# Performance work log

Measured on AMD Instinct MI355X. Metric: run time of the kernel, lower is better.

## Reference

```python
import jax, jax.numpy as jnp
import numpy as np

H, W = 200, 200            # image_size
X_RANGE = (0.0, 100.0)
Y_RANGE = (0.0, 100.0)
SIZE = 36                   # kernel 'size' from source
SIGMA = 3.0
K = SIZE + 1                # kernel is 37x37 (arange(-18, 19))


def _gaussian_kernel():
    r = jnp.arange(-(SIZE // 2), SIZE // 2 + 1, dtype=jnp.float32)
    k1 = jnp.exp(-(r ** 2) / (2.0 * SIGMA ** 2))
    k2 = k1[:, None] * k1[None, :]
    return k2 / k2.sum()    # [K, K]


def setup_inputs() -> dict:
    key = jax.random.key(0)
    # trajectory coords in world units [0, 100) -> spread over whole map
    x_t = jax.random.uniform(key, (512, 64, 2), dtype=jnp.float32) * 100.0
    return {"x_t": x_t}


def reference(x_t):
    B, T, _ = x_t.shape
    x_scale = W / (X_RANGE[1] - X_RANGE[0])
    y_scale = H / (Y_RANGE[1] - Y_RANGE[0])
    # .long() in torch truncates toward zero; inputs are >= 0 here so astype(int32) matches
    x_pix = ((x_t[:, :, 0] - X_RANGE[0]) * x_scale).astype(jnp.int32)   # [B, T]
    y_pix = H - ((x_t[:, :, 1] - Y_RANGE[0]) * y_scale).astype(jnp.int32)
    valid = ~(jnp.isnan(x_t[:, :, 0]) | jnp.isnan(x_t[:, :, 1]))        # [B, T]

    half = SIZE // 2
    x_start = jnp.clip(x_pix - half, 0, W - SIZE)
    y_start = jnp.clip(y_pix - half, 0, H - SIZE)
    x_end = jnp.clip(x_pix + half, 0, W)
    y_end = jnp.clip(y_pix + half, 0, H)
    kx = x_end - x_start    # patch width  (<= 36, kernel[:,:kx] = top-left slice)
    ky = y_end - y_start    # patch height

    kern = _gaussian_kernel()                       # [K, K]
    r = jnp.arange(K)
    c = jnp.arange(K)
    # mask: kernel[:ky, :kx] slice, and point validity            [B, T, K, K]
    mask = ((r[None, None, :, None] < ky[..., None, None])
            & (c[None, None, None, :] < kx[..., None, None])
            & valid[..., None, None])
    vals = jnp.where(mask, kern[None, None, :, :], 0.0)            # [B, T, K, K]
    rows = jnp.clip(y_start[..., None, None] + r[None, None, :, None], 0, H - 1)
    cols = jnp.clip(x_start[..., None, None] + c[None, None, None, :], 0, W - 1)
    rows = jnp.broadcast_to(rows, (B, T, K, K))
    cols = jnp.broadcast_to(cols, (B, T, K, K))
    flat = (rows * W + cols).reshape(B, -1)                        # [B, T*K*K]

    # parallel scatter-add splat of all Gaussian patches
    heat = jnp.zeros((B, H * W), jnp.float32)
    heat = heat.at[jnp.arange(B)[:, None], flat].add(vals.reshape(B, -1))
    heat = heat.reshape(B, H, W)

    # per-image max normalization (max over dim1 then dim2 == max over both)
    m = heat.max(axis=(1, 2), keepdims=True)
    return heat / (m + 1e-10)
```

## Files before the change

### kernel.cpp

```cpp
#include <hip/hip_runtime.h>


#define NT 64
#define BLK 512
#define TDIM 224
#define NTL 7

typedef short bf16x8 __attribute__((ext_vector_type(8)));
typedef float f32x16 __attribute__((ext_vector_type(16)));

static __device__ inline unsigned short f2bf(float f) {
    unsigned int u = __float_as_uint(f);
    u = (u + 0x7FFFu + ((u >> 16) & 1u)) >> 16;
    return (unsigned short)u;
}

struct __align__(16) SMem {
    unsigned short Rm[TDIM][64];
    unsigned short Cm[TDIM][64];
    unsigned short k1b[40];
    float wmax[8];
};

__global__ __launch_bounds__(BLK, 4) void heatmap_kernel(const float* __restrict__ x_t,
                                                         float* __restrict__ out) {
    __shared__ SMem s;
    const int tid  = threadIdx.x;
    const int lane = tid & 63;
    const int wv   = tid >> 6;
    const int b    = blockIdx.x;

    if (tid < 37) {
        float sum = 0.0f, mine = 0.0f;
        #pragma unroll
        for (int i = 0; i < 37; ++i) {
            float r = (float)(i - 18);
            float v = expf(-(r * r) * (1.0f / 18.0f));
            sum += v;
            if (i == tid) mine = v;
        }
        s.k1b[tid] = f2bf(mine / sum);
    }
    __syncthreads();

    {
        const int q  = tid & 31;
        const int r0 = tid >> 5;
        float4 pxy = *(const float4*)(x_t + (size_t)b * NT * 2 + 4 * q);
        bool v0 = (pxy.x == pxy.x) && (pxy.y == pxy.y);
        int xp0 = (int)(pxy.x * 2.0f), yp0 = 200 - (int)(pxy.y * 2.0f);
        int xs0 = min(max(xp0 - 18, 0), 164), ys0 = min(max(yp0 - 18, 0), 164);
        int kx0 = v0 ? (min(max(xp0 + 18, 0), 200) - xs0) : 0;
        int ky0 = v0 ? (min(max(yp0 + 18, 0), 200) - ys0) : 0;
        bool v1 = (pxy.z == pxy.z) && (pxy.w == pxy.w);
        int xp1 = (int)(pxy.z * 2.0f), yp1 = 200 - (int)(pxy.w * 2.0f);
        int xs1 = min(max(xp1 - 18, 0), 164), ys1 = min(max(yp1 - 18, 0), 164);
        int kx1 = v1 ? (min(max(xp1 + 18, 0), 200) - xs1) : 0;
        int ky1 = v1 ? (min(max(yp1 + 18, 0), 200) - ys1) : 0;

        for (int i = 0; i < TDIM / 16; ++i) {
            int row = r0 + 16 * i;
            int sw  = (4 * q) ^ ((row & 7) << 4);
            int d0 = row - ys0, d1 = row - ys1;
            unsigned a0 = ((unsigned)d0 < (unsigned)ky0) ? s.k1b[d0] : 0u;
            unsigned a1 = ((unsigned)d1 < (unsigned)ky1) ? s.k1b[d1] : 0u;
            *(unsigned*)((char*)s.Rm + row * 128 + sw) = a0 | (a1 << 16);
            int e0 = row - xs0, e1 = row - xs1;
            unsigned c0 = ((unsigned)e0 < (unsigned)kx0) ? s.k1b[e0] : 0u;
            unsigned c1 = ((unsigned)e1 < (unsigned)kx1) ? s.k1b[e1] : 0u;
            *(unsigned*)((char*)s.Cm + row * 128 + sw) = c0 | (c1 << 16);
        }
    }
    __syncthreads();

    const int ty  = wv;
    const int swl = (lane & 7) << 4;
    bf16x8 A[4];
    if (ty < NTL) {
        const char* ab = (const char*)s.Rm + (ty * 32 + (lane & 31)) * 128;
        #pragma unroll
        for (int m = 0; m < 4; ++m)
            A[m] = *(const bf16x8*)(ab + ((16 * (2 * m + (lane >> 5))) ^ swl));
    }

    float gmax = 0.0f;
    if (ty < NTL) {
        for (int tx = 0; tx < NTL; ++tx) {
            const char* bb = (const char*)s.Cm + (tx * 32 + (lane & 31)) * 128;
            f32x16 acc;
            #pragma unroll
            for (int r = 0; r < 16; ++r) acc[r] = 0.0f;
            #pragma unroll
            for (int m = 0; m < 4; ++m) {
                bf16x8 B = *(const bf16x8*)(bb + ((16 * (2 * m + (lane >> 5))) ^ swl));
                acc = __builtin_amdgcn_mfma_f32_32x32x16_bf16(A[m], B, acc, 0, 0, 0);
            }
            #pragma unroll
            for (int r = 0; r < 16; ++r) gmax = fmaxf(gmax, acc[r]);
        }
    }
    #pragma unroll
    for (int off = 32; off > 0; off >>= 1) gmax = fmaxf(gmax, __shfl_xor(gmax, off));
    if (lane == 0) s.wmax[wv] = gmax;
    __syncthreads();
    float mm = s.wmax[0];
    #pragma unroll
    for (int w = 1; w < 8; ++w) mm = fmaxf(mm, s.wmax[w]);
    const float scale = 1.0f / (mm + 1e-10f);

    if (ty < NTL) {
        float* ob = out + (size_t)b * (200 * 200);
        for (int tx = 0; tx < NTL; ++tx) {
            const char* bb = (const char*)s.Cm + (tx * 32 + (lane & 31)) * 128;
            f32x16 acc;
            #pragma unroll
            for (int r = 0; r < 16; ++r) acc[r] = 0.0f;
            #pragma unroll
            for (int m = 0; m < 4; ++m) {
                bf16x8 B = *(const bf16x8*)(bb + ((16 * (2 * m + (lane >> 5))) ^ swl));
                acc = __builtin_amdgcn_mfma_f32_32x32x16_bf16(A[m], B, acc, 0, 0, 0);
            }
            const int gcol = tx * 32 + (lane & 31);
            #pragma unroll
            for (int r = 0; r < 16; ++r) {
                int grow = ty * 32 + (r & 3) + 8 * (r >> 2) + 4 * (lane >> 5);
                if (grow < 200 && gcol < 200)
                    ob[grow * 200 + gcol] = acc[r] * scale;
            }
        }
    }
}

extern "C" void kernel_launch(void* const* d_in, const int* in_sizes, int n_in,
                              void* d_out, int out_size, void* d_ws, size_t ws_size,
                              hipStream_t stream) {
    const float* x_t = (const float*)d_in[0];
    float* out = (float*)d_out;
    const int B = in_sizes[0] / (NT * 2);
    heatmap_kernel<<<B, BLK, 0, stream>>>(x_t, out);
}
```

Before: 24.90 us.

## Split heatmap into max-reduction kernel and row-tiled store kernel

The single fused kernel is replaced by two launches. The first computes the per-image maximum with 448 threads (no idle wave) and writes it to workspace. The second launches B×7 blocks, each recomputing its row-band's 1-D factors and the column factors and storing one 32-row tile. This spreads the output-store phase across more blocks to raise parallelism. In exchange it adds a second launch, redundant factor construction per block, and a workspace round trip.

```diff
diff --git a/kernel.cpp b/kernel.cpp
--- a/kernel.cpp
+++ b/kernel.cpp
@@ -2,7 +2,6 @@
 
 
 #define NT 64
-#define BLK 512
 #define TDIM 224
 #define NTL 7
 
@@ -15,21 +14,23 @@
     return (unsigned short)u;
 }
 
-struct __align__(16) SMem {
-    unsigned short Rm[TDIM][64];
-    unsigned short Cm[TDIM][64];
-    unsigned short k1b[40];
-    float wmax[8];
-};
-
-__global__ __launch_bounds__(BLK, 4) void heatmap_kernel(const float* __restrict__ x_t,
-                                                         float* __restrict__ out) {
-    __shared__ SMem s;
-    const int tid  = threadIdx.x;
-    const int lane = tid & 63;
-    const int wv   = tid >> 6;
-    const int b    = blockIdx.x;
-
+struct PMeta { int xs0, ys0, kx0, ky0, xs1, ys1, kx1, ky1; };
+static __device__ inline PMeta pmeta(float4 pxy) {
+    PMeta m;
+    bool v0 = (pxy.x == pxy.x) && (pxy.y == pxy.y);
+    int xp0 = (int)(pxy.x * 2.0f), yp0 = 200 - (int)(pxy.y * 2.0f);
+    m.xs0 = min(max(xp0 - 18, 0), 164); m.ys0 = min(max(yp0 - 18, 0), 164);
+    m.kx0 = v0 ? (min(max(xp0 + 18, 0), 200) - m.xs0) : 0;
+    m.ky0 = v0 ? (min(max(yp0 + 18, 0), 200) - m.ys0) : 0;
+    bool v1 = (pxy.z == pxy.z) && (pxy.w == pxy.w);
+    int xp1 = (int)(pxy.z * 2.0f), yp1 = 200 - (int)(pxy.w * 2.0f);
+    m.xs1 = min(max(xp1 - 18, 0), 164); m.ys1 = min(max(yp1 - 18, 0), 164);
+    m.kx1 = v1 ? (min(max(xp1 + 18, 0), 200) - m.xs1) : 0;
+    m.ky1 = v1 ? (min(max(yp1 + 18, 0), 200) - m.ys1) : 0;
+    return m;
+}
+
+static __device__ inline void build_k1b(int tid, unsigned short* k1b) {
     if (tid < 37) {
         float sum = 0.0f, mine = 0.0f;
         #pragma unroll
@@ -39,78 +40,143 @@
             sum += v;
             if (i == tid) mine = v;
         }
-        s.k1b[tid] = f2bf(mine / sum);
-    }
+        k1b[tid] = f2bf(mine / sum);
+    }
+}
+
+struct __align__(16) SMemA {
+    unsigned short Rm[TDIM][64];
+    unsigned short Cm[TDIM][64];
+    unsigned short k1b[40];
+    float wmax[NTL];
+};
+
+__global__ __launch_bounds__(448) void max_kernel(const float* __restrict__ x_t,
+                                                  float* __restrict__ wsmax) {
+    __shared__ SMemA s;
+    const int tid  = threadIdx.x;
+    const int lane = tid & 63;
+    const int wv   = tid >> 6;
+    const int b    = blockIdx.x;
+
+    build_k1b(tid, s.k1b);
     __syncthreads();
 
     {
         const int q  = tid & 31;
         const int r0 = tid >> 5;
-        float4 pxy = *(const float4*)(x_t + (size_t)b * NT * 2 + 4 * q);
-        bool v0 = (pxy.x == pxy.x) && (pxy.y == pxy.y);
-        int xp0 = (int)(pxy.x * 2.0f), yp0 = 200 - (int)(pxy.y * 2.0f);
-        int xs0 = min(max(xp0 - 18, 0), 164), ys0 = min(max(yp0 - 18, 0), 164);
-        int kx0 = v0 ? (min(max(xp0 + 18, 0), 200) - xs0) : 0;
-        int ky0 = v0 ? (min(max(yp0 + 18, 0), 200) - ys0) : 0;
-        bool v1 = (pxy.z == pxy.z) && (pxy.w == pxy.w);
-        int xp1 = (int)(pxy.z * 2.0f), yp1 = 200 - (int)(pxy.w * 2.0f);
-        int xs1 = min(max(xp1 - 18, 0), 164), ys1 = min(max(yp1 - 18, 0), 164);
-        int kx1 = v1 ? (min(max(xp1 + 18, 0), 200) - xs1) : 0;
-        int ky1 = v1 ? (min(max(yp1 + 18, 0), 200) - ys1) : 0;
-
-        for (int i = 0; i < TDIM / 16; ++i) {
-            int row = r0 + 16 * i;
+        PMeta m = pmeta(*(const float4*)(x_t + (size_t)b * NT * 2 + 4 * q));
+        #pragma unroll
+        for (int i = 0; i < 16; ++i) {
+            int row = r0 + 14 * i;
             int sw  = (4 * q) ^ ((row & 7) << 4);
-            int d0 = row - ys0, d1 = row - ys1;
-            unsigned a0 = ((unsigned)d0 < (unsigned)ky0) ? s.k1b[d0] : 0u;
-            unsigned a1 = ((unsigned)d1 < (unsigned)ky1) ? s.k1b[d1] : 0u;
+            int d0 = row - m.ys0, d1 = row - m.ys1;
+            unsigned a0 = ((unsigned)d0 < (unsigned)m.ky0) ? s.k1b[d0] : 0u;
+            unsigned a1 = ((unsigned)d1 < (unsigned)m.ky1) ? s.k1b[d1] : 0u;
             *(unsigned*)((char*)s.Rm + row * 128 + sw) = a0 | (a1 << 16);
-            int e0 = row - xs0, e1 = row - xs1;
-            unsigned c0 = ((unsigned)e0 < (unsigned)kx0) ? s.k1b[e0] : 0u;
-            unsigned c1 = ((unsigned)e1 < (unsigned)kx1) ? s.k1b[e1] : 0u;
+            int e0 = row - m.xs0, e1 = row - m.xs1;
+            unsigned c0 = ((unsigned)e0 < (unsigned)m.kx0) ? s.k1b[e0] : 0u;
+            unsigned c1 = ((unsigned)e1 < (unsigned)m.kx1) ? s.k1b[e1] : 0u;
             *(unsigned*)((char*)s.Cm + row * 128 + sw) = c0 | (c1 << 16);
         }
     }
     __syncthreads();
 
-    const int ty  = wv;
     const int swl = (lane & 7) << 4;
     bf16x8 A[4];
-    if (ty < NTL) {
-        const char* ab = (const char*)s.Rm + (ty * 32 + (lane & 31)) * 128;
+    {
+        const char* ab = (const char*)s.Rm + (wv * 32 + (lane & 31)) * 128;
         #pragma unroll
         for (int m = 0; m < 4; ++m)
             A[m] = *(const bf16x8*)(ab + ((16 * (2 * m + (lane >> 5))) ^ swl));
     }
 
     float gmax = 0.0f;
-    if (ty < NTL) {
-        for (int tx = 0; tx < NTL; ++tx) {
-            const char* bb = (const char*)s.Cm + (tx * 32 + (lane & 31)) * 128;
-            f32x16 acc;
-            #pragma unroll
-            for (int r = 0; r < 16; ++r) acc[r] = 0.0f;
-            #pragma unroll
-            for (int m = 0; m < 4; ++m) {
-                bf16x8 B = *(const bf16x8*)(bb + ((16 * (2 * m + (lane >> 5))) ^ swl));
-                acc = __builtin_amdgcn_mfma_f32_32x32x16_bf16(A[m], B, acc, 0, 0, 0);
-            }
-            #pragma unroll
-            for (int r = 0; r < 16; ++r) gmax = fmaxf(gmax, acc[r]);
-        }
+    for (int tx = 0; tx < NTL; ++tx) {
+        const char* bb = (const char*)s.Cm + (tx * 32 + (lane & 31)) * 128;
+        f32x16 acc;
+        #pragma unroll
+        for (int r = 0; r < 16; ++r) acc[r] = 0.0f;
+        #pragma unroll
+        for (int m = 0; m < 4; ++m) {
+            bf16x8 B = *(const bf16x8*)(bb + ((16 * (2 * m + (lane >> 5))) ^ swl));
+            acc = __builtin_amdgcn_mfma_f32_32x32x16_bf16(A[m], B, acc, 0, 0, 0);
+        }
+        #pragma unroll
+        for (int r = 0; r < 16; ++r) gmax = fmaxf(gmax, acc[r]);
     }
     #pragma unroll
     for (int off = 32; off > 0; off >>= 1) gmax = fmaxf(gmax, __shfl_xor(gmax, off));
     if (lane == 0) s.wmax[wv] = gmax;
     __syncthreads();
-    float mm = s.wmax[0];
+    if (tid == 0) {
+        float mm = s.wmax[0];
+        #pragma unroll
+        for (int w = 1; w < NTL; ++w) mm = fmaxf(mm, s.wmax[w]);
+        wsmax[b] = mm;
+    }
+}
+
+struct __align__(16) SMemB {
+    unsigned short Cm[TDIM][64];
+    unsigned short Rm[32][64];
+    unsigned short k1b[40];
+};
+
+__global__ __launch_bounds__(256) void store_kernel(const float* __restrict__ x_t,
+                                                    const float* __restrict__ wsmax,
+                                                    float* __restrict__ out) {
+    __shared__ SMemB s;
+    const int tid  = threadIdx.x;
+    const int lane = tid & 63;
+    const int wv   = tid >> 6;
+    const int b    = blockIdx.x;
+    const int ty   = blockIdx.y;
+
+    build_k1b(tid, s.k1b);
+    __syncthreads();
+
+    {
+        const int q  = tid & 31;
+        const int r0 = tid >> 5;
+        PMeta m = pmeta(*(const float4*)(x_t + (size_t)b * NT * 2 + 4 * q));
+        #pragma unroll
+        for (int i = 0; i < 28; ++i) {
+            int row = r0 + 8 * i;
+            int sw  = (4 * q) ^ ((row & 7) << 4);
+            int e0 = row - m.xs0, e1 = row - m.xs1;
+            unsigned c0 = ((unsigned)e0 < (unsigned)m.kx0) ? s.k1b[e0] : 0u;
+            unsigned c1 = ((unsigned)e1 < (unsigned)m.kx1) ? s.k1b[e1] : 0u;
+            *(unsigned*)((char*)s.Cm + row * 128 + sw) = c0 | (c1 << 16);
+        }
+        #pragma unroll
+        for (int i = 0; i < 4; ++i) {
+            int lr  = r0 + 8 * i;
+            int row = 32 * ty + lr;
+            int sw  = (4 * q) ^ ((lr & 7) << 4);
+            int d0 = row - m.ys0, d1 = row - m.ys1;
+            unsigned a0 = ((unsigned)d0 < (unsigned)m.ky0) ? s.k1b[d0] : 0u;
+            unsigned a1 = ((unsigned)d1 < (unsigned)m.ky1) ? s.k1b[d1] : 0u;
+            *(unsigned*)((char*)s.Rm + lr * 128 + sw) = a0 | (a1 << 16);
+        }
+    }
+    __syncthreads();
+
+    const float scale = 1.0f / (wsmax[b] + 1e-10f);
+    const int swl = (lane & 7) << 4;
+    bf16x8 A[4];
+    {
+        const char* ab = (const char*)s.Rm + (lane & 31) * 128;
+        #pragma unroll
+        for (int m = 0; m < 4; ++m)
+            A[m] = *(const bf16x8*)(ab + ((16 * (2 * m + (lane >> 5))) ^ swl));
+    }
+
+    float* ob = out + (size_t)b * (200 * 200);
     #pragma unroll
-    for (int w = 1; w < 8; ++w) mm = fmaxf(mm, s.wmax[w]);
-    const float scale = 1.0f / (mm + 1e-10f);
-
-    if (ty < NTL) {
-        float* ob = out + (size_t)b * (200 * 200);
-        for (int tx = 0; tx < NTL; ++tx) {
+    for (int t = 0; t < 2; ++t) {
+        const int tx = wv + 4 * t;
+        if (tx < NTL) {
             const char* bb = (const char*)s.Cm + (tx * 32 + (lane & 31)) * 128;
             f32x16 acc;
             #pragma unroll
@@ -123,7 +189,7 @@
             const int gcol = tx * 32 + (lane & 31);
             #pragma unroll
             for (int r = 0; r < 16; ++r) {
-                int grow = ty * 32 + (r & 3) + 8 * (r >> 2) + 4 * (lane >> 5);
+                int grow = 32 * ty + (r & 3) + 8 * (r >> 2) + 4 * (lane >> 5);
                 if (grow < 200 && gcol < 200)
                     ob[grow * 200 + gcol] = acc[r] * scale;
             }
@@ -136,6 +202,8 @@
                               hipStream_t stream) {
     const float* x_t = (const float*)d_in[0];
     float* out = (float*)d_out;
+    float* wsmax = (float*)d_ws;
     const int B = in_sizes[0] / (NT * 2);
-    heatmap_kernel<<<B, BLK, 0, stream>>>(x_t, out);
-}
+    max_kernel<<<B, 448, 0, stream>>>(x_t, wsmax);
+    store_kernel<<<dim3(B, NTL), 256, 0, stream>>>(x_t, wsmax, out);
+}
```

Measured after the change: 38.24 us. +53.5%, slower.
